# Performance work log

Measured on AMD Instinct MI355X. Metric: run time of the kernel, lower is better.

Reference implementation:

```python
import jax, jax.numpy as jnp
import numpy as np

N, E, D, H, C = 100000, 1600000, 128, 128, 40


def _sage_conv(x, src, dst, Wl, bl, Wr):
    # mean-aggregate source features into destinations, then dual linear
    n = x.shape[0]
    agg = jax.ops.segment_sum(x[src], dst, num_segments=n)          # [N, D]
    cnt = jax.ops.segment_sum(jnp.ones((src.shape[0],), x.dtype), dst, num_segments=n)
    mean = agg / jnp.maximum(cnt, 1.0)[:, None]
    return mean @ Wl.T + bl + x @ Wr.T                               # [N, H]


def setup_inputs() -> dict:
    key = jax.random.key(0)
    ks = jax.random.split(key, 10)
    s = 1.0 / np.sqrt(D)
    return {
        "x": jax.random.normal(ks[0], (N, D), dtype=jnp.float32),
        "edge_index": jax.random.randint(ks[1], (2, E), 0, N, dtype=jnp.int64),
        "Wl1": jax.random.uniform(ks[2], (H, D), jnp.float32, -s, s),
        "bl1": jnp.zeros((H,), jnp.float32),
        "Wr1": jax.random.uniform(ks[3], (H, D), jnp.float32, -s, s),
        "Wl2": jax.random.uniform(ks[4], (H, H), jnp.float32, -s, s),
        "bl2": jnp.zeros((H,), jnp.float32),
        "Wr2": jax.random.uniform(ks[5], (H, H), jnp.float32, -s, s),
        "Wout": jax.random.uniform(ks[6], (C, H), jnp.float32, -s, s),
        "bout": jnp.zeros((C,), jnp.float32),
    }


def reference(x, edge_index, Wl1, bl1, Wr1, Wl2, bl2, Wr2, Wout, bout):
    src, dst = edge_index[0], edge_index[1]
    h = jax.nn.relu(_sage_conv(x, src, dst, Wl1, bl1, Wr1))   # dropout is identity in eval
    h = jax.nn.relu(_sage_conv(h, src, dst, Wl2, bl2, Wr2))
    return h @ Wout.T + bout                                   # [N, C] logits
```

## Files before the change

kernel.cpp:

```cpp
#include <hip/hip_runtime.h>

#define NN 100000
#define DD 128
#define CC 40
#define BSH 9
#define BSZ 512
#define NBK ((NN + BSZ - 1) / BSZ)
#define CAPT 10240
#define CAPP (CAPT + 3 * BSZ)

typedef unsigned int  uint;
typedef unsigned short ushort;

typedef __attribute__((ext_vector_type(8))) short  s16x8;
typedef __attribute__((ext_vector_type(4))) float  f32x4;
typedef __attribute__((ext_vector_type(4))) uint   u32x4;

__device__ __forceinline__ float blo(uint u) { return __uint_as_float(u << 16); }
__device__ __forceinline__ float bhi(uint u) { return __uint_as_float(u & 0xFFFF0000u); }
__device__ __forceinline__ uint  f2b(float f) {
    uint u = __float_as_uint(f);
    return (u + 0x7FFFu + ((u >> 16) & 1u)) >> 16;
}
__device__ __forceinline__ uint pack2(float lo, float hi) { return f2b(lo) | (f2b(hi) << 16); }

__global__ __launch_bounds__(256)
void k_cvt(const float* __restrict__ x, uint* __restrict__ xh,
           uint* __restrict__ h1, int n8) {
    int i = blockIdx.x * 256 + threadIdx.x;
    if (i < 16) {
        u32x4 z = {0, 0, 0, 0};
        reinterpret_cast<u32x4*>(xh + (size_t)NN * 64)[i] = z;
        reinterpret_cast<u32x4*>(h1 + (size_t)NN * 64)[i] = z;
    }
    if (i >= n8) return;
    float4 a = reinterpret_cast<const float4*>(x)[i * 2];
    float4 b = reinterpret_cast<const float4*>(x)[i * 2 + 1];
    uint4 o;
    o.x = pack2(a.x, a.y); o.y = pack2(a.z, a.w);
    o.z = pack2(b.x, b.y); o.w = pack2(b.z, b.w);
    reinterpret_cast<uint4*>(xh)[i] = o;
}

__global__ __launch_bounds__(256)
void k_prepw(const float* __restrict__ Wl1, const float* __restrict__ Wr1,
             const float* __restrict__ Wl2, const float* __restrict__ Wr2,
             const float* __restrict__ Wout,
             uint* __restrict__ pB1, uint* __restrict__ pB2,
             uint* __restrict__ pBout) {
    int t = blockIdx.x * 256 + threadIdx.x;
    if (t < 8192) {
        int layer = t >> 12;
        int r = t & 4095;
        int kb = r >> 9, nt = (r >> 6) & 7, l = r & 63;
        int n  = nt * 16 + (l & 15);
        int k0 = kb * 32 + ((l >> 4) << 3);
        const float* W = (k0 < 128) ? (layer ? Wl2 : Wl1) : (layer ? Wr2 : Wr1);
        int kk = k0 & 127;
        float4 wa = *reinterpret_cast<const float4*>(W + n * DD + kk);
        float4 wb = *reinterpret_cast<const float4*>(W + n * DD + kk + 4);
        uint4 o;
        o.x = pack2(wa.x, wa.y); o.y = pack2(wa.z, wa.w);
        o.z = pack2(wb.x, wb.y); o.w = pack2(wb.z, wb.w);
        uint* pB = layer ? pB2 : pB1;
        *reinterpret_cast<uint4*>(pB + (size_t)r * 4) = o;
    } else if (t < 8960) {
        int r = t - 8192;
        int kb = r / 192, rem = r % 192;
        int nt = rem >> 6, l = rem & 63;
        int n  = nt * 16 + (l & 15);
        int k0 = kb * 32 + ((l >> 4) << 3);
        uint4 o = {0, 0, 0, 0};
        if (n < CC) {
            float4 wa = *reinterpret_cast<const float4*>(Wout + n * DD + k0);
            float4 wb = *reinterpret_cast<const float4*>(Wout + n * DD + k0 + 4);
            o.x = pack2(wa.x, wa.y); o.y = pack2(wa.z, wa.w);
            o.z = pack2(wb.x, wb.y); o.w = pack2(wb.z, wb.w);
        }
        *reinterpret_cast<uint4*>(pBout + (size_t)r * 4) = o;
    }
}

__global__ __launch_bounds__(256)
void k_partition(const int* __restrict__ src, const int* __restrict__ dst,
                 int* __restrict__ bcur, uint* __restrict__ tmp, int E) {
    __shared__ int h[NBK];
    __shared__ int cur[NBK];
    int chunk = (E + gridDim.x - 1) / gridDim.x;
    int lo = blockIdx.x * chunk;
    int hi = min(lo + chunk, E);
    for (int i = threadIdx.x; i < NBK; i += 256) h[i] = 0;
    __syncthreads();
    for (int i = lo + threadIdx.x; i < hi; i += 256)
        atomicAdd(&h[dst[i] >> BSH], 1);
    __syncthreads();
    for (int i = threadIdx.x; i < NBK; i += 256) {
        int c = h[i];
        cur[i] = c ? atomicAdd(&bcur[i], c) : 0;
    }
    __syncthreads();
    for (int i = lo + threadIdx.x; i < hi; i += 256) {
        int d = dst[i];
        int bkt = d >> BSH;
        int rel = atomicAdd(&cur[bkt], 1);
        if (rel < CAPT)
            tmp[(size_t)bkt * CAPT + rel] =
                ((uint)(d & (BSZ - 1)) << 17) | (uint)src[i];
    }
}

__global__ __launch_bounds__(256)
void k_bucket(const uint* __restrict__ tmp, const int* __restrict__ bcnt,
              int2* __restrict__ rowinfo, int* __restrict__ adj) {
    __shared__ int cnt[BSZ];
    __shared__ int cur[BSZ];
    __shared__ int ps[256];
    int b = blockIdx.x, t = threadIdx.x;
    int count = min(bcnt[b], CAPT);
    const uint* tb = tmp + (size_t)b * CAPT;
    int bbP = b * CAPP;
    cnt[t] = 0; cnt[t + 256] = 0;
    __syncthreads();
    for (int i = t; i < count; i += 256)
        atomicAdd(&cnt[tb[i] >> 17], 1);
    __syncthreads();
    int c0 = cnt[2 * t], c1 = cnt[2 * t + 1];
    int p0 = (c0 + 3) & ~3, p1 = (c1 + 3) & ~3;
    ps[t] = p0 + p1;
    __syncthreads();
    for (int off = 1; off < 256; off <<= 1) {
        int add = (t >= off) ? ps[t - off] : 0;
        __syncthreads();
        ps[t] += add;
        __syncthreads();
    }
    int ex = ps[t] - (p0 + p1);
    cur[2 * t] = ex; cur[2 * t + 1] = ex + p0;
    int node0 = b * BSZ;
    if (node0 + 2 * t < NN)     rowinfo[node0 + 2 * t]     = make_int2(bbP + ex, c0);
    if (node0 + 2 * t + 1 < NN) rowinfo[node0 + 2 * t + 1] = make_int2(bbP + ex + p0, c1);
    __syncthreads();
    for (int i = t; i < count; i += 256) {
        uint e = tb[i];
        int pos = bbP + atomicAdd(&cur[e >> 17], 1);
        adj[pos] = (int)(e & 0x1FFFFu);
    }
    __syncthreads();
    for (int q = c0; q < p0; ++q) adj[bbP + ex + q] = NN;
    int ex1 = ex + p0;
    for (int q = c1; q < p1; ++q) adj[bbP + ex1 + q] = NN;
}

__global__ __launch_bounds__(256)
void k_aggregate(const int2* __restrict__ rowinfo, const int* __restrict__ adj,
                 const uint* __restrict__ xh, uint* __restrict__ outm) {
    const int lane = threadIdx.x & 63;
    const int w = blockIdx.x * 4 + __builtin_amdgcn_readfirstlane(threadIdx.x >> 6);
    int2 ri = rowinfo[w];
    const int beg = __builtin_amdgcn_readfirstlane(ri.x);
    const int n   = __builtin_amdgcn_readfirstlane(ri.y);
    const int end = beg + ((n + 3) & ~3);
    const uint co = (uint)((lane & 31) << 1);

    float a0 = 0.f, a1 = 0.f, a2 = 0.f, a3 = 0.f;
    float b0 = 0.f, b1 = 0.f, b2 = 0.f, b3 = 0.f;

    int j = beg;
    #pragma unroll 2
    for (; j + 8 <= end; j += 8) {
        int4 nA = *reinterpret_cast<const int4*>(adj + j);
        int4 nB = *reinterpret_cast<const int4*>(adj + j + 4);
        int r0 = (lane < 32) ? nA.x : nA.y;
        int r1 = (lane < 32) ? nA.z : nA.w;
        int r2 = (lane < 32) ? nB.x : nB.y;
        int r3 = (lane < 32) ? nB.z : nB.w;
        uint2 v0 = *reinterpret_cast<const uint2*>(xh + ((uint)r0 << 6) + co);
        uint2 v1 = *reinterpret_cast<const uint2*>(xh + ((uint)r1 << 6) + co);
        uint2 v2 = *reinterpret_cast<const uint2*>(xh + ((uint)r2 << 6) + co);
        uint2 v3 = *reinterpret_cast<const uint2*>(xh + ((uint)r3 << 6) + co);
        a0 += blo(v0.x); a1 += bhi(v0.x); a2 += blo(v0.y); a3 += bhi(v0.y);
        b0 += blo(v1.x); b1 += bhi(v1.x); b2 += blo(v1.y); b3 += bhi(v1.y);
        a0 += blo(v2.x); a1 += bhi(v2.x); a2 += blo(v2.y); a3 += bhi(v2.y);
        b0 += blo(v3.x); b1 += bhi(v3.x); b2 += blo(v3.y); b3 += bhi(v3.y);
    }
    if (j < end) {
        int4 nA = *reinterpret_cast<const int4*>(adj + j);
        int r0 = (lane < 32) ? nA.x : nA.y;
        int r1 = (lane < 32) ? nA.z : nA.w;
        uint2 v0 = *reinterpret_cast<const uint2*>(xh + ((uint)r0 << 6) + co);
        uint2 v1 = *reinterpret_cast<const uint2*>(xh + ((uint)r1 << 6) + co);
        a0 += blo(v0.x); a1 += bhi(v0.x); a2 += blo(v0.y); a3 += bhi(v0.y);
        b0 += blo(v1.x); b1 += bhi(v1.x); b2 += blo(v1.y); b3 += bhi(v1.y);
    }

    float t0 = a0 + b0, t1 = a1 + b1, t2 = a2 + b2, t3 = a3 + b3;
    t0 += __shfl_xor(t0, 32);
    t1 += __shfl_xor(t1, 32);
    t2 += __shfl_xor(t2, 32);
    t3 += __shfl_xor(t3, 32);
    if (lane < 32) {
        float inv = 1.0f / fmaxf((float)n, 1.0f);
        uint2 o;
        o.x = pack2(t0 * inv, t1 * inv);
        o.y = pack2(t2 * inv, t3 * inv);
        *reinterpret_cast<uint2*>(outm + (uint)(w * 64) + ((uint)lane << 1)) = o;
    }
}

template <bool HEAD>
__global__ __launch_bounds__(256)
void k_linear_t(const ushort* __restrict__ mean, const ushort* __restrict__ xin,
                const uint* __restrict__ pB, const float* __restrict__ bias,
                ushort* __restrict__ outh,
                const uint* __restrict__ pBout, const float* __restrict__ bout,
                float* __restrict__ outf)
{
    __shared__ u32x4 sB[4096];
    const int tid = threadIdx.x;
    const u32x4* pBv = reinterpret_cast<const u32x4*>(pB);
    #pragma unroll
    for (int i = 0; i < 16; ++i)
        sB[tid + i * 256] = pBv[tid + i * 256];

    const int w = tid >> 6, l = tid & 63;
    const int fq = l >> 4, fr = l & 15;
    const int rbase = blockIdx.x * 128 + w * 32;

    f32x4 acc[2][8] = {};
    __syncthreads();

    #pragma unroll
    for (int kb = 0; kb < 8; ++kb) {
        const ushort* In = (kb < 4) ? mean : xin;
        const int ko = (kb & 3) * 32 + fq * 8;
        s16x8 a0 = __builtin_bit_cast(s16x8,
            *reinterpret_cast<const u32x4*>(In + (size_t)(rbase + fr) * DD + ko));
        s16x8 a1 = __builtin_bit_cast(s16x8,
            *reinterpret_cast<const u32x4*>(In + (size_t)(rbase + 16 + fr) * DD + ko));
        #pragma unroll
        for (int nt = 0; nt < 8; ++nt) {
            s16x8 b = __builtin_bit_cast(s16x8, sB[(kb * 8 + nt) * 64 + l]);
            acc[0][nt] = __builtin_amdgcn_mfma_f32_16x16x32_bf16(a0, b, acc[0][nt], 0, 0, 0);
            acc[1][nt] = __builtin_amdgcn_mfma_f32_16x16x32_bf16(a1, b, acc[1][nt], 0, 0, 0);
        }
    }

    __syncthreads();
    ushort* sH = reinterpret_cast<ushort*>(sB);
    const int LDH = 136;
    #pragma unroll
    for (int nt = 0; nt < 8; ++nt) {
        float bn = bias[nt * 16 + fr];
        #pragma unroll
        for (int m = 0; m < 2; ++m) {
            #pragma unroll
            for (int reg = 0; reg < 4; ++reg) {
                int lrow = w * 32 + m * 16 + fq * 4 + reg;
                float o = fmaxf(acc[m][nt][reg] + bn, 0.0f);
                sH[lrow * LDH + nt * 16 + fr] = (ushort)f2b(o);
            }
        }
    }
    __syncthreads();

    if constexpr (!HEAD) {
        #pragma unroll
        for (int k2 = 0; k2 < 8; ++k2) {
            int idx = k2 * 256 + tid;
            int row = idx >> 4, seg = idx & 15;
            int gr = blockIdx.x * 128 + row;
            if (gr < NN) {
                u32x4 v = *reinterpret_cast<const u32x4*>(sH + row * LDH + seg * 8);
                *reinterpret_cast<u32x4*>(outh + (size_t)gr * DD + seg * 8) = v;
            }
        }
    } else {
        f32x4 oa[2][3] = {};
        #pragma unroll
        for (int kb2 = 0; kb2 < 4; ++kb2) {
            s16x8 a0 = *reinterpret_cast<const s16x8*>(
                sH + (w * 32 + fr) * LDH + kb2 * 32 + fq * 8);
            s16x8 a1 = *reinterpret_cast<const s16x8*>(
                sH + (w * 32 + 16 + fr) * LDH + kb2 * 32 + fq * 8);
            #pragma unroll
            for (int nt2 = 0; nt2 < 3; ++nt2) {
                s16x8 b = __builtin_bit_cast(s16x8,
                    *reinterpret_cast<const u32x4*>(
                        pBout + (size_t)((kb2 * 3 + nt2) * 64 + l) * 4));
                oa[0][nt2] = __builtin_amdgcn_mfma_f32_16x16x32_bf16(a0, b, oa[0][nt2], 0, 0, 0);
                oa[1][nt2] = __builtin_amdgcn_mfma_f32_16x16x32_bf16(a1, b, oa[1][nt2], 0, 0, 0);
            }
        }
        #pragma unroll
        for (int nt2 = 0; nt2 < 3; ++nt2) {
            int col = nt2 * 16 + fr;
            if (col < CC) {
                float bn = bout[col];
                #pragma unroll
                for (int m = 0; m < 2; ++m) {
                    #pragma unroll
                    for (int reg = 0; reg < 4; ++reg) {
                        int r = rbase + m * 16 + fq * 4 + reg;
                        if (r < NN)
                            outf[(size_t)r * CC + col] = oa[m][nt2][reg] + bn;
                    }
                }
            }
        }
    }
}

extern "C" void kernel_launch(void* const* d_in, const int* in_sizes, int n_in,
                              void* d_out, int out_size, void* d_ws, size_t ws_size,
                              hipStream_t stream)
{
    const float* x    = (const float*)d_in[0];
    const int*   ei   = (const int*)d_in[1];
    const float* Wl1  = (const float*)d_in[2];
    const float* bl1  = (const float*)d_in[3];
    const float* Wr1  = (const float*)d_in[4];
    const float* Wl2  = (const float*)d_in[5];
    const float* bl2  = (const float*)d_in[6];
    const float* Wr2  = (const float*)d_in[7];
    const float* Wout = (const float*)d_in[8];
    const float* bout = (const float*)d_in[9];
    float* out = (float*)d_out;

    const int E = in_sizes[1] / 2;
    const int* srcI = ei;
    const int* dstI = ei + E;

    ushort* xh = (ushort*)d_ws;
    ushort* m  = xh + (size_t)(NN + 1) * DD;
    ushort* h1 = m + (size_t)NN * DD;
    int2* rowinfo = (int2*)(h1 + (size_t)(NN + 1) * DD);
    int* adj  = (int*)(rowinfo + NN);
    uint* tmp = (uint*)(adj + (size_t)NBK * CAPP);
    int* bcur = (int*)(tmp + (size_t)NBK * CAPT);
    uintptr_t pb = ((uintptr_t)(bcur + NBK) + 15) & ~(uintptr_t)15;
    uint* pB1   = (uint*)pb;
    uint* pB2   = pB1 + 16384;
    uint* pBout = pB2 + 16384;

    dim3 b256(256);
    const int aggBlocks = NN / 4;
    const int linBlocks = (NN + 127) / 128;
    const int n8 = NN * DD / 8;

    k_cvt<<<(n8 + 255) / 256, b256, 0, stream>>>(x, (uint*)xh, (uint*)h1, n8);
    k_prepw<<<35, b256, 0, stream>>>(Wl1, Wr1, Wl2, Wr2, Wout, pB1, pB2, pBout);
    hipMemsetAsync(bcur, 0, NBK * sizeof(int), stream);
    k_partition<<<256, b256, 0, stream>>>(srcI, dstI, bcur, tmp, E);
    k_bucket<<<NBK, b256, 0, stream>>>(tmp, bcur, rowinfo, adj);

    k_aggregate<<<aggBlocks, b256, 0, stream>>>(rowinfo, adj, (const uint*)xh, (uint*)m);
    k_linear_t<false><<<linBlocks, b256, 0, stream>>>(m, xh, pB1, bl1, h1,
                                                      nullptr, nullptr, nullptr);

    k_aggregate<<<aggBlocks, b256, 0, stream>>>(rowinfo, adj, (const uint*)h1, (uint*)m);
    k_linear_t<true><<<linBlocks, b256, 0, stream>>>(m, h1, pB2, bl2, nullptr,
                                                     pBout, bout, out);
}
```

Before: 217.8 us.

## Split bf16 features into 8 column chunks for cache-resident chunked aggregation

Stores node features (x, h1, mean) as 8 column chunks of 16 bf16 each, so every chunk is a contiguous array of about 3.2 MB. The aggregation kernel now runs each chunk in separate blocks, with one wave gathering 8 neighbors per step at 32 bytes per neighbor. Each wave handles 8 nodes in turn. The aim is to keep each chunk's working set in L2/LLC, which cuts DRAM traffic from random gathers. The cost is 8x re-reading of adjacency lists, narrower 32-byte gather transactions, padding to multiples of 8, and strided A-tile loads in the linear kernel.

```diff
diff --git a/kernel.cpp b/kernel.cpp
--- a/kernel.cpp
+++ b/kernel.cpp
@@ -7,7 +7,9 @@
 #define BSZ 512
 #define NBK ((NN + BSZ - 1) / BSZ)
 #define CAPT 10240
-#define CAPP (CAPT + 3 * BSZ)
+#define CAPP (CAPT + 7 * BSZ)
+#define CS1U ((NN + 1) * 16)
+#define CSMU (NN * 16)
 
 typedef unsigned int  uint;
 typedef unsigned short ushort;
@@ -25,21 +27,25 @@
 __device__ __forceinline__ uint pack2(float lo, float hi) { return f2b(lo) | (f2b(hi) << 16); }
 
 __global__ __launch_bounds__(256)
-void k_cvt(const float* __restrict__ x, uint* __restrict__ xh,
-           uint* __restrict__ h1, int n8) {
+void k_cvt(const float* __restrict__ x, ushort* __restrict__ xh,
+           ushort* __restrict__ h1, int total) {
     int i = blockIdx.x * 256 + threadIdx.x;
     if (i < 16) {
+        int chunk = i >> 1, off = (i & 1) * 8;
         u32x4 z = {0, 0, 0, 0};
-        reinterpret_cast<u32x4*>(xh + (size_t)NN * 64)[i] = z;
-        reinterpret_cast<u32x4*>(h1 + (size_t)NN * 64)[i] = z;
-    }
-    if (i >= n8) return;
-    float4 a = reinterpret_cast<const float4*>(x)[i * 2];
-    float4 b = reinterpret_cast<const float4*>(x)[i * 2 + 1];
+        *reinterpret_cast<u32x4*>(xh + (size_t)chunk * CS1U + (size_t)NN * 16 + off) = z;
+        *reinterpret_cast<u32x4*>(h1 + (size_t)chunk * CS1U + (size_t)NN * 16 + off) = z;
+    }
+    if (i >= total) return;
+    int r = i >> 4, seg = i & 15;
+    const float* xp = x + (size_t)r * DD + seg * 8;
+    float4 a = *reinterpret_cast<const float4*>(xp);
+    float4 b = *reinterpret_cast<const float4*>(xp + 4);
     uint4 o;
     o.x = pack2(a.x, a.y); o.y = pack2(a.z, a.w);
     o.z = pack2(b.x, b.y); o.w = pack2(b.z, b.w);
-    reinterpret_cast<uint4*>(xh)[i] = o;
+    int chunk = seg >> 1, off = (seg & 1) * 8;
+    *reinterpret_cast<uint4*>(xh + (size_t)chunk * CS1U + (size_t)r * 16 + off) = o;
 }
 
 __global__ __launch_bounds__(256)
@@ -125,7 +131,7 @@
         atomicAdd(&cnt[tb[i] >> 17], 1);
     __syncthreads();
     int c0 = cnt[2 * t], c1 = cnt[2 * t + 1];
-    int p0 = (c0 + 3) & ~3, p1 = (c1 + 3) & ~3;
+    int p0 = (c0 + 7) & ~7, p1 = (c1 + 7) & ~7;
     ps[t] = p0 + p1;
     __syncthreads();
     for (int off = 1; off < 256; off <<= 1) {
@@ -153,57 +159,45 @@
 
 __global__ __launch_bounds__(256)
 void k_aggregate(const int2* __restrict__ rowinfo, const int* __restrict__ adj,
-                 const uint* __restrict__ xh, uint* __restrict__ outm) {
-    const int lane = threadIdx.x & 63;
-    const int w = blockIdx.x * 4 + __builtin_amdgcn_readfirstlane(threadIdx.x >> 6);
-    int2 ri = rowinfo[w];
-    const int beg = __builtin_amdgcn_readfirstlane(ri.x);
-    const int n   = __builtin_amdgcn_readfirstlane(ri.y);
-    const int end = beg + ((n + 3) & ~3);
-    const uint co = (uint)((lane & 31) << 1);
-
-    float a0 = 0.f, a1 = 0.f, a2 = 0.f, a3 = 0.f;
-    float b0 = 0.f, b1 = 0.f, b2 = 0.f, b3 = 0.f;
-
-    int j = beg;
-    #pragma unroll 2
-    for (; j + 8 <= end; j += 8) {
-        int4 nA = *reinterpret_cast<const int4*>(adj + j);
-        int4 nB = *reinterpret_cast<const int4*>(adj + j + 4);
-        int r0 = (lane < 32) ? nA.x : nA.y;
-        int r1 = (lane < 32) ? nA.z : nA.w;
-        int r2 = (lane < 32) ? nB.x : nB.y;
-        int r3 = (lane < 32) ? nB.z : nB.w;
-        uint2 v0 = *reinterpret_cast<const uint2*>(xh + ((uint)r0 << 6) + co);
-        uint2 v1 = *reinterpret_cast<const uint2*>(xh + ((uint)r1 << 6) + co);
-        uint2 v2 = *reinterpret_cast<const uint2*>(xh + ((uint)r2 << 6) + co);
-        uint2 v3 = *reinterpret_cast<const uint2*>(xh + ((uint)r3 << 6) + co);
-        a0 += blo(v0.x); a1 += bhi(v0.x); a2 += blo(v0.y); a3 += bhi(v0.y);
-        b0 += blo(v1.x); b1 += bhi(v1.x); b2 += blo(v1.y); b3 += bhi(v1.y);
-        a0 += blo(v2.x); a1 += bhi(v2.x); a2 += blo(v2.y); a3 += bhi(v2.y);
-        b0 += blo(v3.x); b1 += bhi(v3.x); b2 += blo(v3.y); b3 += bhi(v3.y);
-    }
-    if (j < end) {
-        int4 nA = *reinterpret_cast<const int4*>(adj + j);
-        int r0 = (lane < 32) ? nA.x : nA.y;
-        int r1 = (lane < 32) ? nA.z : nA.w;
-        uint2 v0 = *reinterpret_cast<const uint2*>(xh + ((uint)r0 << 6) + co);
-        uint2 v1 = *reinterpret_cast<const uint2*>(xh + ((uint)r1 << 6) + co);
-        a0 += blo(v0.x); a1 += bhi(v0.x); a2 += blo(v0.y); a3 += bhi(v0.y);
-        b0 += blo(v1.x); b1 += bhi(v1.x); b2 += blo(v1.y); b3 += bhi(v1.y);
-    }
-
-    float t0 = a0 + b0, t1 = a1 + b1, t2 = a2 + b2, t3 = a3 + b3;
-    t0 += __shfl_xor(t0, 32);
-    t1 += __shfl_xor(t1, 32);
-    t2 += __shfl_xor(t2, 32);
-    t3 += __shfl_xor(t3, 32);
-    if (lane < 32) {
-        float inv = 1.0f / fmaxf((float)n, 1.0f);
-        uint2 o;
-        o.x = pack2(t0 * inv, t1 * inv);
-        o.y = pack2(t2 * inv, t3 * inv);
-        *reinterpret_cast<uint2*>(outm + (uint)(w * 64) + ((uint)lane << 1)) = o;
+                 const uint* __restrict__ xsrc, uint xsu,
+                 uint* __restrict__ outm) {
+    const int tid = threadIdx.x;
+    const int lane = tid & 63;
+    const int chunk = blockIdx.x & 7;
+    const int nbase = (blockIdx.x >> 3) * 32 + (tid >> 6) * 8;
+    const uint s = (uint)(lane >> 3), f = (uint)(lane & 7);
+    const uint* __restrict__ xc = xsrc + (size_t)chunk * xsu;
+    uint* __restrict__ oc = outm + (size_t)chunk * (NN * 8);
+
+    for (int nn = 0; nn < 8; ++nn) {
+        const int node = nbase + nn;
+        int2 ri = rowinfo[node];
+        const int beg = __builtin_amdgcn_readfirstlane(ri.x);
+        const int n   = __builtin_amdgcn_readfirstlane(ri.y);
+        const int end = beg + ((n + 7) & ~7);
+        float a0 = 0.f, a1 = 0.f, b0 = 0.f, b1 = 0.f;
+        int j = beg;
+        for (; j + 16 <= end; j += 16) {
+            int r0 = __builtin_nontemporal_load(adj + j + s);
+            int r1 = __builtin_nontemporal_load(adj + j + 8 + s);
+            uint v0 = xc[(uint)r0 * 8u + f];
+            uint v1 = xc[(uint)r1 * 8u + f];
+            a0 += blo(v0); a1 += bhi(v0);
+            b0 += blo(v1); b1 += bhi(v1);
+        }
+        if (j < end) {
+            int r0 = __builtin_nontemporal_load(adj + j + s);
+            uint v0 = xc[(uint)r0 * 8u + f];
+            a0 += blo(v0); a1 += bhi(v0);
+        }
+        a0 += b0; a1 += b1;
+        a0 += __shfl_xor(a0, 8);  a1 += __shfl_xor(a1, 8);
+        a0 += __shfl_xor(a0, 16); a1 += __shfl_xor(a1, 16);
+        a0 += __shfl_xor(a0, 32); a1 += __shfl_xor(a1, 32);
+        if (lane < 8) {
+            float inv = 1.0f / fmaxf((float)n, 1.0f);
+            oc[(uint)node * 8u + f] = pack2(a0 * inv, a1 * inv);
+        }
     }
 }
 
@@ -232,11 +226,13 @@
     #pragma unroll
     for (int kb = 0; kb < 8; ++kb) {
         const ushort* In = (kb < 4) ? mean : xin;
+        const uint cs    = (kb < 4) ? (uint)CSMU : (uint)CS1U;
         const int ko = (kb & 3) * 32 + fq * 8;
+        const ushort* pa = In + (size_t)(ko >> 4) * cs + (ko & 8);
         s16x8 a0 = __builtin_bit_cast(s16x8,
-            *reinterpret_cast<const u32x4*>(In + (size_t)(rbase + fr) * DD + ko));
+            *reinterpret_cast<const u32x4*>(pa + (size_t)(rbase + fr) * 16));
         s16x8 a1 = __builtin_bit_cast(s16x8,
-            *reinterpret_cast<const u32x4*>(In + (size_t)(rbase + 16 + fr) * DD + ko));
+            *reinterpret_cast<const u32x4*>(pa + (size_t)(rbase + 16 + fr) * 16));
         #pragma unroll
         for (int nt = 0; nt < 8; ++nt) {
             s16x8 b = __builtin_bit_cast(s16x8, sB[(kb * 8 + nt) * 64 + l]);
@@ -271,7 +267,8 @@
             int gr = blockIdx.x * 128 + row;
             if (gr < NN) {
                 u32x4 v = *reinterpret_cast<const u32x4*>(sH + row * LDH + seg * 8);
-                *reinterpret_cast<u32x4*>(outh + (size_t)gr * DD + seg * 8) = v;
+                *reinterpret_cast<u32x4*>(outh + (size_t)(seg >> 1) * CS1U +
+                                          (size_t)gr * 16 + (seg & 1) * 8) = v;
             }
         }
     } else {
@@ -331,9 +328,9 @@
     const int* dstI = ei + E;
 
     ushort* xh = (ushort*)d_ws;
-    ushort* m  = xh + (size_t)(NN + 1) * DD;
-    ushort* h1 = m + (size_t)NN * DD;
-    int2* rowinfo = (int2*)(h1 + (size_t)(NN + 1) * DD);
+    ushort* m  = xh + (size_t)8 * CS1U;
+    ushort* h1 = m + (size_t)8 * CSMU;
+    int2* rowinfo = (int2*)(h1 + (size_t)8 * CS1U);
     int* adj  = (int*)(rowinfo + NN);
     uint* tmp = (uint*)(adj + (size_t)NBK * CAPP);
     int* bcur = (int*)(tmp + (size_t)NBK * CAPT);
@@ -343,21 +340,21 @@
     uint* pBout = pB2 + 16384;
 
     dim3 b256(256);
-    const int aggBlocks = NN / 4;
+    const int aggBlocks = (NN / 32) * 8;
     const int linBlocks = (NN + 127) / 128;
-    const int n8 = NN * DD / 8;
-
-    k_cvt<<<(n8 + 255) / 256, b256, 0, stream>>>(x, (uint*)xh, (uint*)h1, n8);
+    const uint xsu = (uint)((NN + 1) * 8);
+
+    k_cvt<<<(NN * 16 + 255) / 256, b256, 0, stream>>>(x, xh, h1, NN * 16);
     k_prepw<<<35, b256, 0, stream>>>(Wl1, Wr1, Wl2, Wr2, Wout, pB1, pB2, pBout);
     hipMemsetAsync(bcur, 0, NBK * sizeof(int), stream);
     k_partition<<<256, b256, 0, stream>>>(srcI, dstI, bcur, tmp, E);
     k_bucket<<<NBK, b256, 0, stream>>>(tmp, bcur, rowinfo, adj);
 
-    k_aggregate<<<aggBlocks, b256, 0, stream>>>(rowinfo, adj, (const uint*)xh, (uint*)m);
+    k_aggregate<<<aggBlocks, b256, 0, stream>>>(rowinfo, adj, (const uint*)xh, xsu, (uint*)m);
     k_linear_t<false><<<linBlocks, b256, 0, stream>>>(m, xh, pB1, bl1, h1,
                                                       nullptr, nullptr, nullptr);
 
-    k_aggregate<<<aggBlocks, b256, 0, stream>>>(rowinfo, adj, (const uint*)h1, (uint*)m);
+    k_aggregate<<<aggBlocks, b256, 0, stream>>>(rowinfo, adj, (const uint*)h1, xsu, (uint*)m);
     k_linear_t<true><<<linBlocks, b256, 0, stream>>>(m, h1, pB2, bl2, nullptr,
                                                      pBout, bout, out);
 }
```

After: 496.1 us. 128% more time.
